# Kernel optimization log

Hardware: AMD Instinct MI355X
Metric: run time of the kernel (lower is better)

Reference implementation:

```python
import jax, jax.numpy as jnp
import numpy as np

L = 2048      # target/source sequence length (self-attention)
N = 2         # batch size
E = 256       # embed_dim
H = 8         # num_heads
N_AGENTS = 16


def setup_inputs() -> dict:
    key = jax.random.key(0)
    ks = jax.random.split(key, 9)
    w = 0.02
    ids = jax.random.randint(ks[7], (L,), 0, N_AGENTS, dtype=jnp.int32)
    return {
        "query": jax.random.normal(ks[0], (L, N, E), dtype=jnp.float32),
        "in_proj_weight": jax.random.normal(ks[1], (3 * E, E), dtype=jnp.float32) * w,
        "in_proj_bias": jax.random.normal(ks[2], (3 * E,), dtype=jnp.float32) * w,
        "in_proj_weight_self": jax.random.normal(ks[3], (2 * E, E), dtype=jnp.float32) * w,
        "in_proj_bias_self": jax.random.normal(ks[4], (2 * E,), dtype=jnp.float32) * w,
        "out_proj_weight": jax.random.normal(ks[5], (E, E), dtype=jnp.float32) * w,
        "out_proj_bias": jax.random.normal(ks[6], (E,), dtype=jnp.float32) * w,
        "q_identities": ids,                # self-attention: same identities for q and k
        "k_identities": ids,
    }


def reference(query, in_proj_weight, in_proj_bias, in_proj_weight_self,
              in_proj_bias_self, out_proj_weight, out_proj_bias,
              q_identities, k_identities):
    tgt_len, bsz, embed_dim = query.shape
    head_dim = embed_dim // H
    scaling = jnp.asarray(head_dim, query.dtype) ** -0.5

    # combined in-projection (self-attention fast path), then chunk into q,k,v
    qkv = query @ in_proj_weight.T + in_proj_bias            # (L,N,3E)
    q, k, v = jnp.split(qkv, 3, axis=-1)
    qk_self = query @ in_proj_weight_self.T + in_proj_bias_self  # (L,N,2E)
    q_self, k_self = jnp.split(qk_self, 2, axis=-1)

    q = q * scaling
    q_self = q_self * scaling

    def to_heads(x):  # (L,N,E) -> (N*H, L, head_dim), matching torch view+transpose
        return x.reshape(tgt_len, bsz * H, head_dim).transpose(1, 0, 2)

    q, k, v, q_self, k_self = map(to_heads, (q, k, v, q_self, k_self))

    w_inter = jnp.einsum('bld,bsd->bls', q, k)           # (N*H, L, S)
    w_self = jnp.einsum('bld,bsd->bls', q_self, k_self)  # (N*H, L, S)

    # agent-aware mask: 1 where query/key identities match, broadcast over batch*heads
    mask = (k_identities[None, :] == q_identities[:, None]).astype(query.dtype)  # (L,S)
    attn_weights = w_inter * (1.0 - mask) + w_self * mask

    attn = jax.nn.softmax(attn_weights, axis=-1)
    out = jnp.einsum('bls,bsd->bld', attn, v)            # (N*H, L, head_dim)
    out = out.transpose(1, 0, 2).reshape(tgt_len, bsz, embed_dim)
    out = out @ out_proj_weight.T + out_proj_bias        # (L,N,E)
    return out
```

## Files before the change

### kernel.cpp

```cpp
#include <hip/hip_runtime.h>
#include <hip/hip_bf16.h>

typedef __attribute__((ext_vector_type(8))) short short8b;
typedef __attribute__((ext_vector_type(4))) float float4v;

static __device__ __forceinline__ unsigned short f2bf_bits(float f) {
  union { __hip_bfloat16 h; unsigned short u; } c;
  c.h = __float2bfloat16(f);
  return c.u;
}

static __device__ __forceinline__ short8b cvt8(const float* s) {
  union { short8b v; unsigned short us[8]; } o;
#pragma unroll
  for (int i = 0; i < 8; ++i) o.us[i] = f2bf_bits(s[i]);
  return o.v;
}

__global__ __launch_bounds__(256) void cast_X(const float* __restrict__ src,
                                              __hip_bfloat16* __restrict__ dst) {
  int i = blockIdx.x * 256 + threadIdx.x;
  float4 v = reinterpret_cast<const float4*>(src)[i];
  union { ushort4 u; __hip_bfloat16 h[4]; } o;
  o.h[0] = __float2bfloat16(v.x); o.h[1] = __float2bfloat16(v.y);
  o.h[2] = __float2bfloat16(v.z); o.h[3] = __float2bfloat16(v.w);
  reinterpret_cast<ushort4*>(dst)[i] = o.u;
}

__global__ __launch_bounds__(256) void proj_gemm(
    const __hip_bfloat16* __restrict__ Xb, const float* __restrict__ W1,
    const float* __restrict__ W2,
    const float* __restrict__ bias, const float* __restrict__ bias_s,
    __hip_bfloat16* __restrict__ Qs, __hip_bfloat16* __restrict__ Kg,
    __hip_bfloat16* __restrict__ Vt, __hip_bfloat16* __restrict__ Qf,
    __hip_bfloat16* __restrict__ Kf) {
    __shared__ __hip_bfloat16 At[128][40];
    __shared__ __hip_bfloat16 Bt[64][40];
    const int tid = threadIdx.x;
    const int lane = tid & 63, w = tid >> 6;
    const int ln = lane & 15, kg = lane >> 4;
    const int wr = w >> 1, wc = w & 1;
    const int rowBase = blockIdx.y * 128;
    const int colBase = blockIdx.x * 64;
    const float* Wsrc = (colBase < 768) ? (W1 + (size_t)colBase * 256)
                                        : (W2 + (size_t)(colBase - 768) * 256);
    float4v acc[4][2] = {};

    for (int kt = 0; kt < 8; ++kt) {
        int cid = tid;
#pragma unroll
        for (int p = 0; p < 2; ++p, cid += 256) {
            int row = cid >> 2, c = cid & 3;
            *(short8b*)&At[row][c * 8] =
                *(const short8b*)&Xb[(size_t)(rowBase + row) * 256 + kt * 32 + c * 8];
        }
        {
            int row = tid >> 2, c = tid & 3;
            float fb[8];
            *(float4*)&fb[0] = *(const float4*)&Wsrc[(size_t)row * 256 + kt * 32 + c * 8];
            *(float4*)&fb[4] = *(const float4*)&Wsrc[(size_t)row * 256 + kt * 32 + c * 8 + 4];
            *(short8b*)&Bt[row][c * 8] = cvt8(fb);
        }
        __syncthreads();
        short8b a[4], b[2];
#pragma unroll
        for (int mi = 0; mi < 4; ++mi) a[mi] = *(const short8b*)&At[wr * 64 + mi * 16 + ln][kg * 8];
#pragma unroll
        for (int nj = 0; nj < 2; ++nj) b[nj] = *(const short8b*)&Bt[wc * 32 + nj * 16 + ln][kg * 8];
#pragma unroll
        for (int mi = 0; mi < 4; ++mi)
#pragma unroll
            for (int nj = 0; nj < 2; ++nj)
                acc[mi][nj] = __builtin_amdgcn_mfma_f32_16x16x32_bf16(a[mi], b[nj], acc[mi][nj], 0, 0, 0);
        __syncthreads();
    }

    const float scaling = 0.17677669529663687f * 1.4426950408889634f;
#pragma unroll
    for (int mi = 0; mi < 4; ++mi) {
#pragma unroll
        for (int nj = 0; nj < 2; ++nj) {
            int j = colBase + wc * 32 + nj * 16 + ln;
            float bj = (j < 768) ? bias[j] : bias_s[j - 768];
#pragma unroll
            for (int r = 0; r < 4; ++r) {
                int row = rowBase + wr * 64 + mi * 16 + kg * 4 + r;
                float val = acc[mi][nj][r] + bj;
                int l = row >> 1, n = row & 1;
                if (j < 256) {
                    int h = j >> 5, d = j & 31;
                    Qs[(((n << 3) + h) * 2048 + l) * 32 + d] = __float2bfloat16(val * scaling);
                } else if (j < 512) {
                    int e = j - 256, h = e >> 5, d = e & 31;
                    Kg[(((n << 3) + h) * 2048 + l) * 32 + d] = __float2bfloat16(val);
                } else if (j < 768) {
                    int e = j - 512, h = e >> 5, d = e & 31;
                    Vt[(((n << 3) + h) * 32 + d) * 2048 + l] = __float2bfloat16(val);
                } else if (j < 1024) {
                    int e = j - 768, h = e >> 5, d = e & 31;
                    Qf[(((n << 3) + h) * 2048 + l) * 32 + d] = __float2bfloat16(val * scaling);
                } else {
                    int e = j - 1024, h = e >> 5, d = e & 31;
                    Kf[(((n << 3) + h) * 2048 + l) * 32 + d] = __float2bfloat16(val);
                }
            }
        }
    }
}

__global__ __launch_bounds__(256, 2) void agent_attn(
    const __hip_bfloat16* __restrict__ Qs, const __hip_bfloat16* __restrict__ Kg,
    const __hip_bfloat16* __restrict__ Vt, const __hip_bfloat16* __restrict__ Qf,
    const __hip_bfloat16* __restrict__ Kf, const int* __restrict__ qid_g,
    const int* __restrict__ kid_g, float* __restrict__ PO, float* __restrict__ PL) {
  __shared__ __hip_bfloat16 Klds[2][64][36];
  __shared__ __hip_bfloat16 Kslds[2][64][36];
  __shared__ __hip_bfloat16 Vlds[2][32][72];

  const int tid = threadIdx.x;
  const int lane = tid & 63, w = tid >> 6;
  const int ln = lane & 15, kg = lane >> 4;

  const int flat = blockIdx.x;
  const int slot = flat >> 3;
  const int bh = ((flat & 7) << 1) | (slot & 1);
  const int rest = slot >> 1;
  const int qg = rest & 31, split = rest >> 5;
  const int q0 = qg * 64 + w * 16;
  const int kbase = split * 1024;

  const __hip_bfloat16* Qb  = Qs + (size_t)bh * 2048 * 32;
  const __hip_bfloat16* Qfb = Qf + (size_t)bh * 2048 * 32;
  const __hip_bfloat16* Kb  = Kg + (size_t)bh * 2048 * 32;
  const __hip_bfloat16* Ksb = Kf + (size_t)bh * 2048 * 32;
  const __hip_bfloat16* Vb  = Vt + (size_t)bh * 32 * 2048;

  const int krho = tid >> 2, kseg = tid & 3;
  const int ksub = krho >> 4, ki = krho & 15;
  const int gK = ((ki >> 2) << 3) + (ki & 3) + ((ksub & 1) << 5) + ((ksub >> 1) << 2);
  const int vrow = tid >> 3, vseg = tid & 7;

  short8b bQ  = *(const short8b*)&Qb [(q0 + ln) * 32 + kg * 8];
  short8b bQf = *(const short8b*)&Qfb[(q0 + ln) * 32 + kg * 8];
  const int qidq = qid_g[q0 + ln];

  float lacc = 0.f;
  float4v O0 = {0.f, 0.f, 0.f, 0.f}, O1 = {0.f, 0.f, 0.f, 0.f};

  {
    short8b rk = *(const short8b*)&Kb [(size_t)(kbase + gK) * 32 + kseg * 8];
    short8b rs = *(const short8b*)&Ksb[(size_t)(kbase + gK) * 32 + kseg * 8];
    short8b rv = *(const short8b*)&Vb [(size_t)vrow * 2048 + kbase + vseg * 8];
    *(short8b*)&Klds [0][krho][kseg * 8] = rk;
    *(short8b*)&Kslds[0][krho][kseg * 8] = rs;
    *(short8b*)&Vlds [0][vrow][vseg * 8] = rv;
  }
  __syncthreads();

  short8b rk, rs, rv;
#pragma unroll 1
  for (int t = 0; t < 16; ++t) {
    const int cur = t & 1;
    const int s0 = kbase + t * 64;
    if (t < 15) {
      const int s0n = s0 + 64;
      rk = *(const short8b*)&Kb [(size_t)(s0n + gK) * 32 + kseg * 8];
      rs = *(const short8b*)&Ksb[(size_t)(s0n + gK) * 32 + kseg * 8];
      rv = *(const short8b*)&Vb [(size_t)vrow * 2048 + s0n + vseg * 8];
    }
    const int* ip = kid_g + s0 + kg * 8;
    int4 t0 = *(const int4*)(ip);
    int4 t1 = *(const int4*)(ip + 32);
    int4 t2 = *(const int4*)(ip + 4);
    int4 t3 = *(const int4*)(ip + 36);
    int sd[4][4] = {{t0.x, t0.y, t0.z, t0.w}, {t1.x, t1.y, t1.z, t1.w},
                    {t2.x, t2.y, t2.z, t2.w}, {t3.x, t3.y, t3.z, t3.w}};

    short8b aK[4], aS[4], bV[2][2];
#pragma unroll
    for (int sub = 0; sub < 4; ++sub) {
      aK[sub] = *(const short8b*)&Klds [cur][sub * 16 + ln][kg * 8];
      aS[sub] = *(const short8b*)&Kslds[cur][sub * 16 + ln][kg * 8];
    }
#pragma unroll
    for (int kk = 0; kk < 2; ++kk)
#pragma unroll
      for (int dh = 0; dh < 2; ++dh)
        bV[kk][dh] = *(const short8b*)&Vlds[cur][dh * 16 + ln][kk * 32 + kg * 8];

    float4v ci[4], cs[4];
    float4v z = {0.f, 0.f, 0.f, 0.f};
    __builtin_amdgcn_s_setprio(1);
#pragma unroll
    for (int sub = 0; sub < 4; ++sub) {
      ci[sub] = __builtin_amdgcn_mfma_f32_16x16x32_bf16(aK[sub], bQ,  z, 0, 0, 0);
      cs[sub] = __builtin_amdgcn_mfma_f32_16x16x32_bf16(aS[sub], bQf, z, 0, 0, 0);
    }
    __builtin_amdgcn_s_setprio(0);
    float p[4][4];
#pragma unroll
    for (int sub = 0; sub < 4; ++sub)
#pragma unroll
      for (int r = 0; r < 4; ++r)
        p[sub][r] = exp2f((sd[sub][r] == qidq) ? cs[sub][r] : ci[sub][r]);
    float y0 = (p[0][0] + p[0][1]) + (p[0][2] + p[0][3]);
    float y1 = (p[1][0] + p[1][1]) + (p[1][2] + p[1][3]);
    float y2 = (p[2][0] + p[2][1]) + (p[2][2] + p[2][3]);
    float y3 = (p[3][0] + p[3][1]) + (p[3][2] + p[3][3]);
    lacc += (y0 + y1) + (y2 + y3);
    union { short8b v; unsigned short us[8]; } apk[2];
#pragma unroll
    for (int kk = 0; kk < 2; ++kk) {
      apk[kk].us[0] = f2bf_bits(p[kk][0]);     apk[kk].us[1] = f2bf_bits(p[kk][1]);
      apk[kk].us[2] = f2bf_bits(p[kk][2]);     apk[kk].us[3] = f2bf_bits(p[kk][3]);
      apk[kk].us[4] = f2bf_bits(p[kk + 2][0]); apk[kk].us[5] = f2bf_bits(p[kk + 2][1]);
      apk[kk].us[6] = f2bf_bits(p[kk + 2][2]); apk[kk].us[7] = f2bf_bits(p[kk + 2][3]);
    }
    __builtin_amdgcn_s_setprio(1);
#pragma unroll
    for (int kk = 0; kk < 2; ++kk) {
      O0 = __builtin_amdgcn_mfma_f32_16x16x32_bf16(apk[kk].v, bV[kk][0], O0, 0, 0, 0);
      O1 = __builtin_amdgcn_mfma_f32_16x16x32_bf16(apk[kk].v, bV[kk][1], O1, 0, 0, 0);
    }
    __builtin_amdgcn_s_setprio(0);

    if (t < 15) {
      *(short8b*)&Klds [cur ^ 1][krho][kseg * 8] = rk;
      *(short8b*)&Kslds[cur ^ 1][krho][kseg * 8] = rs;
      *(short8b*)&Vlds [cur ^ 1][vrow][vseg * 8] = rv;
    }
    __syncthreads();
  }

  float ps = lacc;
  ps += __shfl_xor(ps, 16);
  ps += __shfl_xor(ps, 32);
  float* pob = PO + (size_t)(split * 16 + bh) * 2048 * 32;
  float* plb = PL + (size_t)(split * 16 + bh) * 2048;
#pragma unroll
  for (int r = 0; r < 4; ++r) {
    int q = q0 + kg * 4 + r;
    pob[(size_t)q * 32 + ln]      = O0[r];
    pob[(size_t)q * 32 + 16 + ln] = O1[r];
  }
  if (kg == 0) plb[q0 + ln] = ps;
}

__global__ __launch_bounds__(256) void combine_splits(
    const float* __restrict__ PO, const float* __restrict__ PL,
    __hip_bfloat16* __restrict__ Ab) {
  const int blk = blockIdx.x;
  const int bh = blk >> 6;
  const int q = ((blk & 63) << 5) | (threadIdx.x >> 3);
  const int d4 = threadIdx.x & 7;
  const int n = bh >> 3, h = bh & 7;
  float L = PL[(size_t)bh * 2048 + q] + PL[(size_t)(16 + bh) * 2048 + q];
  float inv = 1.f / L;
  float4 a0 = *(const float4*)&PO[((size_t)bh * 2048 + q) * 32 + d4 * 4];
  float4 a1 = *(const float4*)&PO[((size_t)(16 + bh) * 2048 + q) * 32 + d4 * 4];
  union { ushort4 u; __hip_bfloat16 hh[4]; } o;
  o.hh[0] = __float2bfloat16((a0.x + a1.x) * inv);
  o.hh[1] = __float2bfloat16((a0.y + a1.y) * inv);
  o.hh[2] = __float2bfloat16((a0.z + a1.z) * inv);
  o.hh[3] = __float2bfloat16((a0.w + a1.w) * inv);
  *(ushort4*)&Ab[((size_t)q * 2 + n) * 256 + h * 32 + d4 * 4] = o.u;
}

__global__ __launch_bounds__(256) void out_gemm(
    const __hip_bfloat16* __restrict__ A, const float* __restrict__ Wo,
    const float* __restrict__ bias, float* __restrict__ out) {
    __shared__ __hip_bfloat16 At[64][40];
    __shared__ __hip_bfloat16 Bt[64][40];
    const int tid = threadIdx.x;
    const int lane = tid & 63, w = tid >> 6;
    const int ln = lane & 15, kg = lane >> 4;
    const int wr = w >> 1, wc = w & 1;
    const int rowBase = blockIdx.y * 64;
    const int colBase = blockIdx.x * 64;
    float4v acc[2][2] = {};

    for (int kt = 0; kt < 8; ++kt) {
        int row = tid >> 2, c = tid & 3;
        *(short8b*)&At[row][c * 8] =
            *(const short8b*)&A[(size_t)(rowBase + row) * 256 + kt * 32 + c * 8];
        float fb[8];
        *(float4*)&fb[0] = *(const float4*)&Wo[(size_t)(colBase + row) * 256 + kt * 32 + c * 8];
        *(float4*)&fb[4] = *(const float4*)&Wo[(size_t)(colBase + row) * 256 + kt * 32 + c * 8 + 4];
        *(short8b*)&Bt[row][c * 8] = cvt8(fb);
        __syncthreads();
        short8b a[2], b[2];
#pragma unroll
        for (int mi = 0; mi < 2; ++mi) a[mi] = *(const short8b*)&At[wr * 32 + mi * 16 + ln][kg * 8];
#pragma unroll
        for (int nj = 0; nj < 2; ++nj) b[nj] = *(const short8b*)&Bt[wc * 32 + nj * 16 + ln][kg * 8];
#pragma unroll
        for (int mi = 0; mi < 2; ++mi)
#pragma unroll
            for (int nj = 0; nj < 2; ++nj)
                acc[mi][nj] = __builtin_amdgcn_mfma_f32_16x16x32_bf16(a[mi], b[nj], acc[mi][nj], 0, 0, 0);
        __syncthreads();
    }

#pragma unroll
    for (int mi = 0; mi < 2; ++mi) {
#pragma unroll
        for (int nj = 0; nj < 2; ++nj) {
            int j = colBase + wc * 32 + nj * 16 + ln;
            float bj = bias[j];
#pragma unroll
            for (int r = 0; r < 4; ++r) {
                int row = rowBase + wr * 32 + mi * 16 + kg * 4 + r;
                out[row * 256 + j] = acc[mi][nj][r] + bj;
            }
        }
    }
}

extern "C" void kernel_launch(void* const* d_in, const int* in_sizes, int n_in,
                              void* d_out, int out_size, void* d_ws, size_t ws_size,
                              hipStream_t stream) {
    const float* query = (const float*)d_in[0];
    const float* W_in  = (const float*)d_in[1];
    const float* b_in  = (const float*)d_in[2];
    const float* W_s   = (const float*)d_in[3];
    const float* b_s   = (const float*)d_in[4];
    const float* W_o   = (const float*)d_in[5];
    const float* b_o   = (const float*)d_in[6];
    const int*   qids  = (const int*)d_in[7];
    const int*   kids  = (const int*)d_in[8];
    float* out = (float*)d_out;

    __hip_bfloat16* Qs  = (__hip_bfloat16*)d_ws;
    __hip_bfloat16* Kg  = Qs + 16 * 2048 * 32;
    __hip_bfloat16* Vt  = Kg + 16 * 2048 * 32;
    __hip_bfloat16* Qf  = Vt + 16 * 2048 * 32;
    __hip_bfloat16* Kf  = Qf + 16 * 2048 * 32;
    __hip_bfloat16* Ab  = Kf + 16 * 2048 * 32;
    __hip_bfloat16* Xb  = Ab + 4096 * 256;
    float* PO = (float*)(Xb + 4096 * 256);
    float* PL = PO + (size_t)2 * 16 * 2048 * 32;

    cast_X<<<1024, 256, 0, stream>>>(query, Xb);
    proj_gemm<<<dim3(20, 32), 256, 0, stream>>>(Xb, W_in, W_s, b_in, b_s,
                                                Qs, Kg, Vt, Qf, Kf);
    agent_attn<<<1024, 256, 0, stream>>>(Qs, Kg, Vt, Qf, Kf, qids, kids, PO, PL);
    combine_splits<<<1024, 256, 0, stream>>>(PO, PL, Ab);
    out_gemm<<<dim3(4, 64), 256, 0, stream>>>(Ab, W_o, b_o, out);
}
```

Before: 64.88 us.

## Fuse split-combine into out-projection GEMM and transpose V in separate kernel

Removes the combine_splits kernel by having out_gemm load both partial attention outputs and their row sums, normalize them, and convert to bf16 while filling its A tile. It also changes proj_gemm to write V row-major, which gives coalesced stores, and adds a small v2t kernel that transposes V through shared memory into the layout attention expects. The trade-off is that out_gemm now reads fp32 partials redundantly across its 4 column blocks, and an extra launch is added for the transpose.

After: 70.07 us. +8.0%, slower.

```diff
diff --git a/kernel.cpp b/kernel.cpp
--- a/kernel.cpp
+++ b/kernel.cpp
@@ -32,7 +32,7 @@
     const float* __restrict__ W2,
     const float* __restrict__ bias, const float* __restrict__ bias_s,
     __hip_bfloat16* __restrict__ Qs, __hip_bfloat16* __restrict__ Kg,
-    __hip_bfloat16* __restrict__ Vt, __hip_bfloat16* __restrict__ Qf,
+    __hip_bfloat16* __restrict__ Vr, __hip_bfloat16* __restrict__ Qf,
     __hip_bfloat16* __restrict__ Kf) {
     __shared__ __hip_bfloat16 At[128][40];
     __shared__ __hip_bfloat16 Bt[64][40];
@@ -95,7 +95,7 @@
                     Kg[(((n << 3) + h) * 2048 + l) * 32 + d] = __float2bfloat16(val);
                 } else if (j < 768) {
                     int e = j - 512, h = e >> 5, d = e & 31;
-                    Vt[(((n << 3) + h) * 32 + d) * 2048 + l] = __float2bfloat16(val);
+                    Vr[(((n << 3) + h) * 2048 + l) * 32 + d] = __float2bfloat16(val);
                 } else if (j < 1024) {
                     int e = j - 768, h = e >> 5, d = e & 31;
                     Qf[(((n << 3) + h) * 2048 + l) * 32 + d] = __float2bfloat16(val * scaling);
@@ -106,6 +106,28 @@
             }
         }
     }
+}
+
+__global__ __launch_bounds__(256) void v2t(const __hip_bfloat16* __restrict__ Vr,
+                                           __hip_bfloat16* __restrict__ Vt) {
+  __shared__ __hip_bfloat16 T[64][36];
+  const int tid = threadIdx.x;
+  const int bh = blockIdx.x >> 5, st = blockIdx.x & 31;
+  const int s0 = st * 64;
+  {
+    int srow = tid >> 2, c = tid & 3;
+    *(short8b*)&T[srow][c * 8] =
+        *(const short8b*)&Vr[((size_t)bh * 2048 + s0 + srow) * 32 + c * 8];
+  }
+  __syncthreads();
+  {
+    int d = tid >> 3, seg = tid & 7;
+    union { short8b v; unsigned short us[8]; } o;
+#pragma unroll
+    for (int i = 0; i < 8; ++i)
+      o.us[i] = *(const unsigned short*)&T[seg * 8 + i][d];
+    *(short8b*)&Vt[((size_t)bh * 32 + d) * 2048 + s0 + seg * 8] = o.v;
+  }
 }
 
 __global__ __launch_bounds__(256, 2) void agent_attn(
@@ -246,29 +268,10 @@
   if (kg == 0) plb[q0 + ln] = ps;
 }
 
-__global__ __launch_bounds__(256) void combine_splits(
+__global__ __launch_bounds__(256) void out_gemm(
     const float* __restrict__ PO, const float* __restrict__ PL,
-    __hip_bfloat16* __restrict__ Ab) {
-  const int blk = blockIdx.x;
-  const int bh = blk >> 6;
-  const int q = ((blk & 63) << 5) | (threadIdx.x >> 3);
-  const int d4 = threadIdx.x & 7;
-  const int n = bh >> 3, h = bh & 7;
-  float L = PL[(size_t)bh * 2048 + q] + PL[(size_t)(16 + bh) * 2048 + q];
-  float inv = 1.f / L;
-  float4 a0 = *(const float4*)&PO[((size_t)bh * 2048 + q) * 32 + d4 * 4];
-  float4 a1 = *(const float4*)&PO[((size_t)(16 + bh) * 2048 + q) * 32 + d4 * 4];
-  union { ushort4 u; __hip_bfloat16 hh[4]; } o;
-  o.hh[0] = __float2bfloat16((a0.x + a1.x) * inv);
-  o.hh[1] = __float2bfloat16((a0.y + a1.y) * inv);
-  o.hh[2] = __float2bfloat16((a0.z + a1.z) * inv);
-  o.hh[3] = __float2bfloat16((a0.w + a1.w) * inv);
-  *(ushort4*)&Ab[((size_t)q * 2 + n) * 256 + h * 32 + d4 * 4] = o.u;
-}
-
-__global__ __launch_bounds__(256) void out_gemm(
-    const __hip_bfloat16* __restrict__ A, const float* __restrict__ Wo,
-    const float* __restrict__ bias, float* __restrict__ out) {
+    const float* __restrict__ Wo, const float* __restrict__ bias,
+    float* __restrict__ out) {
     __shared__ __hip_bfloat16 At[64][40];
     __shared__ __hip_bfloat16 Bt[64][40];
     const int tid = threadIdx.x;
@@ -279,14 +282,36 @@
     const int colBase = blockIdx.x * 64;
     float4v acc[2][2] = {};
 
+    const int arow = tid >> 2, ac = tid & 3;
+    const int q = (rowBase + arow) >> 1, n8 = ((rowBase + arow) & 1) << 3;
+    float invL[8];
+#pragma unroll
     for (int kt = 0; kt < 8; ++kt) {
-        int row = tid >> 2, c = tid & 3;
-        *(short8b*)&At[row][c * 8] =
-            *(const short8b*)&A[(size_t)(rowBase + row) * 256 + kt * 32 + c * 8];
-        float fb[8];
-        *(float4*)&fb[0] = *(const float4*)&Wo[(size_t)(colBase + row) * 256 + kt * 32 + c * 8];
-        *(float4*)&fb[4] = *(const float4*)&Wo[(size_t)(colBase + row) * 256 + kt * 32 + c * 8 + 4];
-        *(short8b*)&Bt[row][c * 8] = cvt8(fb);
+      float L = PL[(size_t)(n8 + kt) * 2048 + q] + PL[(size_t)(16 + n8 + kt) * 2048 + q];
+      invL[kt] = 1.0f / L;
+    }
+
+    for (int kt = 0; kt < 8; ++kt) {
+        {
+            const float* p0 = PO + ((size_t)(n8 + kt) * 2048 + q) * 32 + ac * 8;
+            const float* p1 = PO + ((size_t)(16 + n8 + kt) * 2048 + q) * 32 + ac * 8;
+            float fa[8];
+            *(float4*)&fa[0] = *(const float4*)(p0);
+            *(float4*)&fa[4] = *(const float4*)(p0 + 4);
+            float4 b0 = *(const float4*)(p1);
+            float4 b1 = *(const float4*)(p1 + 4);
+            fa[0] += b0.x; fa[1] += b0.y; fa[2] += b0.z; fa[3] += b0.w;
+            fa[4] += b1.x; fa[5] += b1.y; fa[6] += b1.z; fa[7] += b1.w;
+#pragma unroll
+            for (int i = 0; i < 8; ++i) fa[i] *= invL[kt];
+            *(short8b*)&At[arow][ac * 8] = cvt8(fa);
+        }
+        {
+            float fb[8];
+            *(float4*)&fb[0] = *(const float4*)&Wo[(size_t)(colBase + arow) * 256 + kt * 32 + ac * 8];
+            *(float4*)&fb[4] = *(const float4*)&Wo[(size_t)(colBase + arow) * 256 + kt * 32 + ac * 8 + 4];
+            *(short8b*)&Bt[arow][ac * 8] = cvt8(fb);
+        }
         __syncthreads();
         short8b a[2], b[2];
 #pragma unroll
@@ -332,18 +357,18 @@
 
     __hip_bfloat16* Qs  = (__hip_bfloat16*)d_ws;
     __hip_bfloat16* Kg  = Qs + 16 * 2048 * 32;
-    __hip_bfloat16* Vt  = Kg + 16 * 2048 * 32;
-    __hip_bfloat16* Qf  = Vt + 16 * 2048 * 32;
+    __hip_bfloat16* Vr  = Kg + 16 * 2048 * 32;
+    __hip_bfloat16* Qf  = Vr + 16 * 2048 * 32;
     __hip_bfloat16* Kf  = Qf + 16 * 2048 * 32;
-    __hip_bfloat16* Ab  = Kf + 16 * 2048 * 32;
-    __hip_bfloat16* Xb  = Ab + 4096 * 256;
+    __hip_bfloat16* Vt  = Kf + 16 * 2048 * 32;
+    __hip_bfloat16* Xb  = Vt + 16 * 2048 * 32;
     float* PO = (float*)(Xb + 4096 * 256);
     float* PL = PO + (size_t)2 * 16 * 2048 * 32;
 
     cast_X<<<1024, 256, 0, stream>>>(query, Xb);
     proj_gemm<<<dim3(20, 32), 256, 0, stream>>>(Xb, W_in, W_s, b_in, b_s,
-                                                Qs, Kg, Vt, Qf, Kf);
+                                                Qs, Kg, Vr, Qf, Kf);
+    v2t<<<512, 256, 0, stream>>>(Vr, Vt);
     agent_attn<<<1024, 256, 0, stream>>>(Qs, Kg, Vt, Qf, Kf, qids, kids, PO, PL);
-    combine_splits<<<1024, 256, 0, stream>>>(PO, PL, Ab);
-    out_gemm<<<dim3(4, 64), 256, 0, stream>>>(Ab, W_o, b_o, out);
-}
+    out_gemm<<<dim3(4, 64), 256, 0, stream>>>(PO, PL, W_o, b_o, out);
+}
```

## Split attention keys four ways, load V directly from global, raise occupancy

Applied to the files above, without the earlier changes.

The key range of the attention kernel is split into four chunks of 512 instead of two of 1024, doubling the grid to 2048 blocks, and combine_splits now sums four partials. The V tile is no longer staged through LDS. Each lane loads its V fragments straight from global memory, which shrinks shared memory use, and launch bounds now request 6 blocks per SM instead of 2. The aim is more parallelism and occupancy, at the cost of doubling the partial-output traffic and issuing uncoalesced per-lane V loads that are not prefetched.

Measured after the change: 236.2 us. +264.0%, slower.

```diff
diff --git a/kernel.cpp b/kernel.cpp
--- a/kernel.cpp
+++ b/kernel.cpp
@@ -108,14 +108,13 @@
     }
 }
 
-__global__ __launch_bounds__(256, 2) void agent_attn(
+__global__ __launch_bounds__(256, 6) void agent_attn(
     const __hip_bfloat16* __restrict__ Qs, const __hip_bfloat16* __restrict__ Kg,
     const __hip_bfloat16* __restrict__ Vt, const __hip_bfloat16* __restrict__ Qf,
     const __hip_bfloat16* __restrict__ Kf, const int* __restrict__ qid_g,
     const int* __restrict__ kid_g, float* __restrict__ PO, float* __restrict__ PL) {
   __shared__ __hip_bfloat16 Klds[2][64][36];
   __shared__ __hip_bfloat16 Kslds[2][64][36];
-  __shared__ __hip_bfloat16 Vlds[2][32][72];
 
   const int tid = threadIdx.x;
   const int lane = tid & 63, w = tid >> 6;
@@ -127,7 +126,7 @@
   const int rest = slot >> 1;
   const int qg = rest & 31, split = rest >> 5;
   const int q0 = qg * 64 + w * 16;
-  const int kbase = split * 1024;
+  const int kbase = split * 512;
 
   const __hip_bfloat16* Qb  = Qs + (size_t)bh * 2048 * 32;
   const __hip_bfloat16* Qfb = Qf + (size_t)bh * 2048 * 32;
@@ -138,7 +137,6 @@
   const int krho = tid >> 2, kseg = tid & 3;
   const int ksub = krho >> 4, ki = krho & 15;
   const int gK = ((ki >> 2) << 3) + (ki & 3) + ((ksub & 1) << 5) + ((ksub >> 1) << 2);
-  const int vrow = tid >> 3, vseg = tid & 7;
 
   short8b bQ  = *(const short8b*)&Qb [(q0 + ln) * 32 + kg * 8];
   short8b bQf = *(const short8b*)&Qfb[(q0 + ln) * 32 + kg * 8];
@@ -150,24 +148,27 @@
   {
     short8b rk = *(const short8b*)&Kb [(size_t)(kbase + gK) * 32 + kseg * 8];
     short8b rs = *(const short8b*)&Ksb[(size_t)(kbase + gK) * 32 + kseg * 8];
-    short8b rv = *(const short8b*)&Vb [(size_t)vrow * 2048 + kbase + vseg * 8];
     *(short8b*)&Klds [0][krho][kseg * 8] = rk;
     *(short8b*)&Kslds[0][krho][kseg * 8] = rs;
-    *(short8b*)&Vlds [0][vrow][vseg * 8] = rv;
   }
   __syncthreads();
 
-  short8b rk, rs, rv;
+  short8b rk, rs;
 #pragma unroll 1
-  for (int t = 0; t < 16; ++t) {
+  for (int t = 0; t < 8; ++t) {
     const int cur = t & 1;
     const int s0 = kbase + t * 64;
-    if (t < 15) {
+    if (t < 7) {
       const int s0n = s0 + 64;
       rk = *(const short8b*)&Kb [(size_t)(s0n + gK) * 32 + kseg * 8];
       rs = *(const short8b*)&Ksb[(size_t)(s0n + gK) * 32 + kseg * 8];
-      rv = *(const short8b*)&Vb [(size_t)vrow * 2048 + s0n + vseg * 8];
-    }
+    }
+    short8b bV[2][2];
+#pragma unroll
+    for (int kk = 0; kk < 2; ++kk)
+#pragma unroll
+      for (int dh = 0; dh < 2; ++dh)
+        bV[kk][dh] = *(const short8b*)&Vb[(dh * 16 + ln) * 2048 + s0 + kk * 32 + kg * 8];
     const int* ip = kid_g + s0 + kg * 8;
     int4 t0 = *(const int4*)(ip);
     int4 t1 = *(const int4*)(ip + 32);
@@ -176,17 +177,12 @@
     int sd[4][4] = {{t0.x, t0.y, t0.z, t0.w}, {t1.x, t1.y, t1.z, t1.w},
                     {t2.x, t2.y, t2.z, t2.w}, {t3.x, t3.y, t3.z, t3.w}};
 
-    short8b aK[4], aS[4], bV[2][2];
+    short8b aK[4], aS[4];
 #pragma unroll
     for (int sub = 0; sub < 4; ++sub) {
       aK[sub] = *(const short8b*)&Klds [cur][sub * 16 + ln][kg * 8];
       aS[sub] = *(const short8b*)&Kslds[cur][sub * 16 + ln][kg * 8];
     }
-#pragma unroll
-    for (int kk = 0; kk < 2; ++kk)
-#pragma unroll
-      for (int dh = 0; dh < 2; ++dh)
-        bV[kk][dh] = *(const short8b*)&Vlds[cur][dh * 16 + ln][kk * 32 + kg * 8];
 
     float4v ci[4], cs[4];
     float4v z = {0.f, 0.f, 0.f, 0.f};
@@ -224,10 +220,9 @@
     }
     __builtin_amdgcn_s_setprio(0);
 
-    if (t < 15) {
+    if (t < 7) {
       *(short8b*)&Klds [cur ^ 1][krho][kseg * 8] = rk;
       *(short8b*)&Kslds[cur ^ 1][krho][kseg * 8] = rs;
-      *(short8b*)&Vlds [cur ^ 1][vrow][vseg * 8] = rv;
     }
     __syncthreads();
   }
@@ -254,15 +249,19 @@
   const int q = ((blk & 63) << 5) | (threadIdx.x >> 3);
   const int d4 = threadIdx.x & 7;
   const int n = bh >> 3, h = bh & 7;
-  float L = PL[(size_t)bh * 2048 + q] + PL[(size_t)(16 + bh) * 2048 + q];
+  float L = 0.f;
+#pragma unroll
+  for (int s = 0; s < 4; ++s) L += PL[(size_t)(s * 16 + bh) * 2048 + q];
   float inv = 1.f / L;
-  float4 a0 = *(const float4*)&PO[((size_t)bh * 2048 + q) * 32 + d4 * 4];
-  float4 a1 = *(const float4*)&PO[((size_t)(16 + bh) * 2048 + q) * 32 + d4 * 4];
+  float4 acc = {0.f, 0.f, 0.f, 0.f};
+#pragma unroll
+  for (int s = 0; s < 4; ++s) {
+    float4 v = *(const float4*)&PO[((size_t)(s * 16 + bh) * 2048 + q) * 32 + d4 * 4];
+    acc.x += v.x; acc.y += v.y; acc.z += v.z; acc.w += v.w;
+  }
   union { ushort4 u; __hip_bfloat16 hh[4]; } o;
-  o.hh[0] = __float2bfloat16((a0.x + a1.x) * inv);
-  o.hh[1] = __float2bfloat16((a0.y + a1.y) * inv);
-  o.hh[2] = __float2bfloat16((a0.z + a1.z) * inv);
-  o.hh[3] = __float2bfloat16((a0.w + a1.w) * inv);
+  o.hh[0] = __float2bfloat16(acc.x * inv); o.hh[1] = __float2bfloat16(acc.y * inv);
+  o.hh[2] = __float2bfloat16(acc.z * inv); o.hh[3] = __float2bfloat16(acc.w * inv);
   *(ushort4*)&Ab[((size_t)q * 2 + n) * 256 + h * 32 + d4 * 4] = o.u;
 }
 
@@ -338,12 +337,12 @@
     __hip_bfloat16* Ab  = Kf + 16 * 2048 * 32;
     __hip_bfloat16* Xb  = Ab + 4096 * 256;
     float* PO = (float*)(Xb + 4096 * 256);
-    float* PL = PO + (size_t)2 * 16 * 2048 * 32;
+    float* PL = PO + (size_t)4 * 16 * 2048 * 32;
 
     cast_X<<<1024, 256, 0, stream>>>(query, Xb);
     proj_gemm<<<dim3(20, 32), 256, 0, stream>>>(Xb, W_in, W_s, b_in, b_s,
                                                 Qs, Kg, Vt, Qf, Kf);
-    agent_attn<<<1024, 256, 0, stream>>>(Qs, Kg, Vt, Qf, Kf, qids, kids, PO, PL);
+    agent_attn<<<2048, 256, 0, stream>>>(Qs, Kg, Vt, Qf, Kf, qids, kids, PO, PL);
     combine_splits<<<1024, 256, 0, stream>>>(PO, PL, Ab);
     out_gemm<<<dim3(4, 64), 256, 0, stream>>>(Ab, W_o, b_o, out);
 }
```

## Process two 16-row query tiles per wave to reuse staged K/V tiles

Applied to the files above, without the earlier changes.

Each wave now handles 32 query rows (two 16-row MFMA tiles) instead of 16, so each block covers 128 queries and the grid halves to 512 blocks. The K, K_self and V tiles loaded into shared memory are reused across twice as many queries, which halves global/LDS staging traffic and barrier overhead per unit of work. The K LDS row pitch also changes from 36 to 40 elements, likely to change bank-conflict behaviour. The cost is more registers per thread and fewer blocks, which may lower occupancy and latency hiding on a 256-CU device.

Result: slower. 66.90 us (+3.1%).

```diff
diff --git a/kernel.cpp b/kernel.cpp
--- a/kernel.cpp
+++ b/kernel.cpp
@@ -113,8 +113,8 @@
     const __hip_bfloat16* __restrict__ Vt, const __hip_bfloat16* __restrict__ Qf,
     const __hip_bfloat16* __restrict__ Kf, const int* __restrict__ qid_g,
     const int* __restrict__ kid_g, float* __restrict__ PO, float* __restrict__ PL) {
-  __shared__ __hip_bfloat16 Klds[2][64][36];
-  __shared__ __hip_bfloat16 Kslds[2][64][36];
+  __shared__ __hip_bfloat16 Klds[2][64][40];
+  __shared__ __hip_bfloat16 Kslds[2][64][40];
   __shared__ __hip_bfloat16 Vlds[2][32][72];
 
   const int tid = threadIdx.x;
@@ -125,8 +125,8 @@
   const int slot = flat >> 3;
   const int bh = ((flat & 7) << 1) | (slot & 1);
   const int rest = slot >> 1;
-  const int qg = rest & 31, split = rest >> 5;
-  const int q0 = qg * 64 + w * 16;
+  const int qg = rest & 15, split = rest >> 4;
+  const int q0 = qg * 128 + w * 32;
   const int kbase = split * 1024;
 
   const __hip_bfloat16* Qb  = Qs + (size_t)bh * 2048 * 32;
@@ -140,12 +140,17 @@
   const int gK = ((ki >> 2) << 3) + (ki & 3) + ((ksub & 1) << 5) + ((ksub >> 1) << 2);
   const int vrow = tid >> 3, vseg = tid & 7;
 
-  short8b bQ  = *(const short8b*)&Qb [(q0 + ln) * 32 + kg * 8];
-  short8b bQf = *(const short8b*)&Qfb[(q0 + ln) * 32 + kg * 8];
-  const int qidq = qid_g[q0 + ln];
-
-  float lacc = 0.f;
-  float4v O0 = {0.f, 0.f, 0.f, 0.f}, O1 = {0.f, 0.f, 0.f, 0.f};
+  short8b bQ[2], bQf[2];
+  int qidq[2];
+#pragma unroll
+  for (int qh = 0; qh < 2; ++qh) {
+    bQ[qh]  = *(const short8b*)&Qb [(q0 + qh * 16 + ln) * 32 + kg * 8];
+    bQf[qh] = *(const short8b*)&Qfb[(q0 + qh * 16 + ln) * 32 + kg * 8];
+    qidq[qh] = qid_g[q0 + qh * 16 + ln];
+  }
+
+  float lacc[2] = {0.f, 0.f};
+  float4v O[2][2] = {};
 
   {
     short8b rk = *(const short8b*)&Kb [(size_t)(kbase + gK) * 32 + kseg * 8];
@@ -188,41 +193,44 @@
       for (int dh = 0; dh < 2; ++dh)
         bV[kk][dh] = *(const short8b*)&Vlds[cur][dh * 16 + ln][kk * 32 + kg * 8];
 
-    float4v ci[4], cs[4];
-    float4v z = {0.f, 0.f, 0.f, 0.f};
-    __builtin_amdgcn_s_setprio(1);
-#pragma unroll
-    for (int sub = 0; sub < 4; ++sub) {
-      ci[sub] = __builtin_amdgcn_mfma_f32_16x16x32_bf16(aK[sub], bQ,  z, 0, 0, 0);
-      cs[sub] = __builtin_amdgcn_mfma_f32_16x16x32_bf16(aS[sub], bQf, z, 0, 0, 0);
-    }
-    __builtin_amdgcn_s_setprio(0);
-    float p[4][4];
-#pragma unroll
-    for (int sub = 0; sub < 4; ++sub)
-#pragma unroll
-      for (int r = 0; r < 4; ++r)
-        p[sub][r] = exp2f((sd[sub][r] == qidq) ? cs[sub][r] : ci[sub][r]);
-    float y0 = (p[0][0] + p[0][1]) + (p[0][2] + p[0][3]);
-    float y1 = (p[1][0] + p[1][1]) + (p[1][2] + p[1][3]);
-    float y2 = (p[2][0] + p[2][1]) + (p[2][2] + p[2][3]);
-    float y3 = (p[3][0] + p[3][1]) + (p[3][2] + p[3][3]);
-    lacc += (y0 + y1) + (y2 + y3);
-    union { short8b v; unsigned short us[8]; } apk[2];
-#pragma unroll
-    for (int kk = 0; kk < 2; ++kk) {
-      apk[kk].us[0] = f2bf_bits(p[kk][0]);     apk[kk].us[1] = f2bf_bits(p[kk][1]);
-      apk[kk].us[2] = f2bf_bits(p[kk][2]);     apk[kk].us[3] = f2bf_bits(p[kk][3]);
-      apk[kk].us[4] = f2bf_bits(p[kk + 2][0]); apk[kk].us[5] = f2bf_bits(p[kk + 2][1]);
-      apk[kk].us[6] = f2bf_bits(p[kk + 2][2]); apk[kk].us[7] = f2bf_bits(p[kk + 2][3]);
-    }
-    __builtin_amdgcn_s_setprio(1);
-#pragma unroll
-    for (int kk = 0; kk < 2; ++kk) {
-      O0 = __builtin_amdgcn_mfma_f32_16x16x32_bf16(apk[kk].v, bV[kk][0], O0, 0, 0, 0);
-      O1 = __builtin_amdgcn_mfma_f32_16x16x32_bf16(apk[kk].v, bV[kk][1], O1, 0, 0, 0);
-    }
-    __builtin_amdgcn_s_setprio(0);
+#pragma unroll
+    for (int qh = 0; qh < 2; ++qh) {
+      float4v ci[4], cs[4];
+      float4v z = {0.f, 0.f, 0.f, 0.f};
+      __builtin_amdgcn_s_setprio(1);
+#pragma unroll
+      for (int sub = 0; sub < 4; ++sub) {
+        ci[sub] = __builtin_amdgcn_mfma_f32_16x16x32_bf16(aK[sub], bQ[qh],  z, 0, 0, 0);
+        cs[sub] = __builtin_amdgcn_mfma_f32_16x16x32_bf16(aS[sub], bQf[qh], z, 0, 0, 0);
+      }
+      __builtin_amdgcn_s_setprio(0);
+      float p[4][4];
+#pragma unroll
+      for (int sub = 0; sub < 4; ++sub)
+#pragma unroll
+        for (int r = 0; r < 4; ++r)
+          p[sub][r] = exp2f((sd[sub][r] == qidq[qh]) ? cs[sub][r] : ci[sub][r]);
+      float y0 = (p[0][0] + p[0][1]) + (p[0][2] + p[0][3]);
+      float y1 = (p[1][0] + p[1][1]) + (p[1][2] + p[1][3]);
+      float y2 = (p[2][0] + p[2][1]) + (p[2][2] + p[2][3]);
+      float y3 = (p[3][0] + p[3][1]) + (p[3][2] + p[3][3]);
+      lacc[qh] += (y0 + y1) + (y2 + y3);
+      union { short8b v; unsigned short us[8]; } apk[2];
+#pragma unroll
+      for (int kk = 0; kk < 2; ++kk) {
+        apk[kk].us[0] = f2bf_bits(p[kk][0]);     apk[kk].us[1] = f2bf_bits(p[kk][1]);
+        apk[kk].us[2] = f2bf_bits(p[kk][2]);     apk[kk].us[3] = f2bf_bits(p[kk][3]);
+        apk[kk].us[4] = f2bf_bits(p[kk + 2][0]); apk[kk].us[5] = f2bf_bits(p[kk + 2][1]);
+        apk[kk].us[6] = f2bf_bits(p[kk + 2][2]); apk[kk].us[7] = f2bf_bits(p[kk + 2][3]);
+      }
+      __builtin_amdgcn_s_setprio(1);
+#pragma unroll
+      for (int kk = 0; kk < 2; ++kk) {
+        O[qh][0] = __builtin_amdgcn_mfma_f32_16x16x32_bf16(apk[kk].v, bV[kk][0], O[qh][0], 0, 0, 0);
+        O[qh][1] = __builtin_amdgcn_mfma_f32_16x16x32_bf16(apk[kk].v, bV[kk][1], O[qh][1], 0, 0, 0);
+      }
+      __builtin_amdgcn_s_setprio(0);
+    }
 
     if (t < 15) {
       *(short8b*)&Klds [cur ^ 1][krho][kseg * 8] = rk;
@@ -232,18 +240,21 @@
     __syncthreads();
   }
 
-  float ps = lacc;
-  ps += __shfl_xor(ps, 16);
-  ps += __shfl_xor(ps, 32);
   float* pob = PO + (size_t)(split * 16 + bh) * 2048 * 32;
   float* plb = PL + (size_t)(split * 16 + bh) * 2048;
 #pragma unroll
-  for (int r = 0; r < 4; ++r) {
-    int q = q0 + kg * 4 + r;
-    pob[(size_t)q * 32 + ln]      = O0[r];
-    pob[(size_t)q * 32 + 16 + ln] = O1[r];
+  for (int qh = 0; qh < 2; ++qh) {
+    float ps = lacc[qh];
+    ps += __shfl_xor(ps, 16);
+    ps += __shfl_xor(ps, 32);
+#pragma unroll
+    for (int r = 0; r < 4; ++r) {
+      int q = q0 + qh * 16 + kg * 4 + r;
+      pob[(size_t)q * 32 + ln]      = O[qh][0][r];
+      pob[(size_t)q * 32 + 16 + ln] = O[qh][1][r];
+    }
+    if (kg == 0) plb[q0 + qh * 16 + ln] = ps;
   }
-  if (kg == 0) plb[q0 + ln] = ps;
 }
 
 __global__ __launch_bounds__(256) void combine_splits(
@@ -343,7 +354,7 @@
     cast_X<<<1024, 256, 0, stream>>>(query, Xb);
     proj_gemm<<<dim3(20, 32), 256, 0, stream>>>(Xb, W_in, W_s, b_in, b_s,
                                                 Qs, Kg, Vt, Qf, Kf);
-    agent_attn<<<1024, 256, 0, stream>>>(Qs, Kg, Vt, Qf, Kf, qids, kids, PO, PL);
+    agent_attn<<<512, 256, 0, stream>>>(Qs, Kg, Vt, Qf, Kf, qids, kids, PO, PL);
     combine_splits<<<1024, 256, 0, stream>>>(PO, PL, Ab);
     out_gemm<<<dim3(4, 64), 256, 0, stream>>>(Ab, W_o, b_o, out);
 }
```
